# Kernel tuning notes

Measured on AMD Instinct MI355X. Metric: run time of the kernel, lower is better.

Reference implementation:

```python
import jax, jax.numpy as jnp
import numpy as np

N_NODES = 100000
N_EDGES = 800000
N_GRAPHS = 4000
EMB = 128      # node_emb_dims
HID = 256      # hidden_dims
FP = 2048      # fingerprint_dims
FIELD_DIMS = {"atom_type": 120, "degree": 12, "charge": 10}


def setup_inputs() -> dict:
    key = jax.random.key(0)
    ks = iter(jax.random.split(key, 40))
    p = lambda shape: jax.random.normal(next(ks), shape, dtype=jnp.float32) * 0.02
    inp = {
        "atom_idx": jax.random.randint(next(ks), (N_NODES,), 0, FIELD_DIMS["atom_type"]),
        "degree_idx": jax.random.randint(next(ks), (N_NODES,), 0, FIELD_DIMS["degree"]),
        "charge_idx": jax.random.randint(next(ks), (N_NODES,), 0, FIELD_DIMS["charge"]),
        "edge_index": jax.random.randint(next(ks), (2, N_EDGES), 0, N_NODES),
        "batch": jnp.sort(jax.random.randint(next(ks), (N_NODES,), 0, N_GRAPHS)),
        "fingerprint": jax.random.normal(next(ks), (N_GRAPHS, FP), dtype=jnp.float32),
        # FFM projector params
        "emb_atom": p((FIELD_DIMS["atom_type"], EMB)),
        "emb_degree": p((FIELD_DIMS["degree"], EMB)),
        "emb_charge": p((FIELD_DIMS["charge"], EMB)),
        "proj_w1": p((3 * EMB, EMB)), "proj_b1": jnp.zeros((EMB,), jnp.float32),
        "proj_w2": p((EMB, EMB)), "proj_b2": jnp.zeros((EMB,), jnp.float32),
        # fingerprint linear
        "fp_w": p((FP, HID)), "fp_b": jnp.zeros((HID,), jnp.float32),
        # GCN layers
        "conv_w0": p((EMB, HID)), "conv_b0": jnp.zeros((HID,), jnp.float32),
        "conv_w1": p((HID, HID)), "conv_b1": jnp.zeros((HID,), jnp.float32),
        "conv_w2": p((HID, HID)), "conv_b2": jnp.zeros((HID,), jnp.float32),
        "conv_w3": p((HID, HID)), "conv_b3": jnp.zeros((HID,), jnp.float32),
        # head
        "lin1_w": p((2 * HID, HID // 2)), "lin1_b": jnp.zeros((HID // 2,), jnp.float32),
        "lin2_w": p((HID // 2, 1)), "lin2_b": jnp.zeros((1,), jnp.float32),
    }
    return inp


def gcn_conv(x, w, b, src, dst, n):
    # PyG GCNConv: linear, add self-loops, symmetric norm, scatter-add at dst, + bias
    xw = x @ w
    loop = jnp.arange(n)
    src_f = jnp.concatenate([src, loop])
    dst_f = jnp.concatenate([dst, loop])
    deg = jax.ops.segment_sum(jnp.ones_like(dst_f, dtype=x.dtype), dst_f, num_segments=n)
    dinv = jax.lax.rsqrt(deg)  # deg >= 1 thanks to self-loops
    norm = dinv[src_f] * dinv[dst_f]                       # [E+N]
    msg = xw[src_f] * norm[:, None]                        # [E+N, HID]
    return jax.ops.segment_sum(msg, dst_f, num_segments=n) + b


def reference(atom_idx, degree_idx, charge_idx, edge_index, batch, fingerprint,
              emb_atom, emb_degree, emb_charge,
              proj_w1, proj_b1, proj_w2, proj_b2, fp_w, fp_b,
              conv_w0, conv_b0, conv_w1, conv_b1, conv_w2, conv_b2, conv_w3, conv_b3,
              lin1_w, lin1_b, lin2_w, lin2_b):
    # FieldAwareFactorizationMachine projector (vectorized over all nodes)
    e = jnp.concatenate([emb_atom[atom_idx], emb_degree[degree_idx], emb_charge[charge_idx]], axis=-1)
    h = jax.nn.relu(e @ proj_w1 + proj_b1) @ proj_w2 + proj_b2   # [N, EMB]
    src, dst = edge_index[0], edge_index[1]
    for w, b in ((conv_w0, conv_b0), (conv_w1, conv_b1), (conv_w2, conv_b2), (conv_w3, conv_b3)):
        h = jax.nn.relu(gcn_conv(h, w, b, src, dst, N_NODES))
    pooled = jax.ops.segment_sum(h, batch, num_segments=N_GRAPHS)  # scatter sum pooling
    fp_emb = fingerprint @ fp_w + fp_b
    z = jnp.concatenate([fp_emb, pooled], axis=-1)                 # [B, 2*HID]
    z = jax.nn.relu(z @ lin1_w + lin1_b)
    return z @ lin2_w + lin2_b                                     # [B, 1]
```

## Files before the change

### kernel.cpp

```cpp
#include <hip/hip_runtime.h>
#include <stdint.h>

#define NN 100000
#define NE 800000
#define NG 4000
#define NBLK ((NN + 255) / 256)

typedef __attribute__((ext_vector_type(8))) short s16x8;
typedef __attribute__((ext_vector_type(4))) float f32x4;

__device__ __forceinline__ float b2f(unsigned short u) {
    return __uint_as_float(((unsigned int)u) << 16);
}
__device__ __forceinline__ unsigned short f2b(float f) {
    unsigned int x = __float_as_uint(f);
    x = x + 0x7FFFu + ((x >> 16) & 1u);
    return (unsigned short)(x >> 16);
}
__device__ __forceinline__ s16x8 cvt8(const float* __restrict__ p) {
    float4 a = *(const float4*)p;
    float4 b = *(const float4*)(p + 4);
    s16x8 r = {(short)f2b(a.x), (short)f2b(a.y), (short)f2b(a.z), (short)f2b(a.w),
               (short)f2b(b.x), (short)f2b(b.y), (short)f2b(b.z), (short)f2b(b.w)};
    return r;
}

__global__ void k_count(const int* __restrict__ dst, int* __restrict__ cnt) {
    int e = blockIdx.x * 256 + threadIdx.x;
    if (e < NE) atomicAdd(&cnt[dst[e]], 1);
}

__global__ void k_dinv(const int* __restrict__ cnt, float* __restrict__ dinv) {
    int n = blockIdx.x * 256 + threadIdx.x;
    if (n < NN) dinv[n] = rsqrtf((float)(cnt[n] + 1));
}

__global__ __launch_bounds__(256) void k_bsum(const int* __restrict__ cnt, int* __restrict__ bsum) {
    __shared__ int s[256];
    int i = blockIdx.x * 256 + threadIdx.x;
    s[threadIdx.x] = (i < NN) ? cnt[i] : 0;
    __syncthreads();
    for (int off = 128; off; off >>= 1) {
        if (threadIdx.x < off) s[threadIdx.x] += s[threadIdx.x + off];
        __syncthreads();
    }
    if (threadIdx.x == 0) bsum[blockIdx.x] = s[0];
}

__global__ __launch_bounds__(512) void k_bscan(const int* __restrict__ bsum, int* __restrict__ bpre) {
    __shared__ int s[512];
    int t = threadIdx.x;
    int v = (t < NBLK) ? bsum[t] : 0;
    s[t] = v;
    __syncthreads();
    for (int off = 1; off < 512; off <<= 1) {
        int u = (t >= off) ? s[t - off] : 0;
        __syncthreads();
        s[t] += u;
        __syncthreads();
    }
    if (t < NBLK) bpre[t] = s[t] - v;
}

__global__ __launch_bounds__(256) void k_rowptr(const int* __restrict__ cnt, const int* __restrict__ bpre,
                                                int* __restrict__ row_ptr, int* __restrict__ cursor) {
    __shared__ int s[256];
    int t = threadIdx.x;
    int i = blockIdx.x * 256 + t;
    int v = (i < NN) ? cnt[i] : 0;
    s[t] = v;
    __syncthreads();
    for (int off = 1; off < 256; off <<= 1) {
        int u = (t >= off) ? s[t - off] : 0;
        __syncthreads();
        s[t] += u;
        __syncthreads();
    }
    if (i < NN) {
        int excl = bpre[blockIdx.x] + s[t] - v;
        row_ptr[i] = excl;
        cursor[i] = excl;
        if (i == NN - 1) row_ptr[NN] = NE;
    }
}

__global__ void k_fill(const int* __restrict__ src, const int* __restrict__ dst,
                       int* __restrict__ cursor, int* __restrict__ colA) {
    int e = blockIdx.x * 256 + threadIdx.x;
    if (e < NE) {
        int d = dst[e];
        int p = atomicAdd(&cursor[d], 1);
        colA[p] = src[e];
    }
}

__global__ void k_t(const float* __restrict__ src, unsigned short* __restrict__ dst, int KN, int ln) {
    int i = blockIdx.x * 256 + threadIdx.x;
    if (i < KN) {
        int k = i >> ln, n = i & ((1 << ln) - 1);
        dst[(size_t)n * (KN >> ln) + k] = f2b(src[i]);
    }
}

__global__ void k_cvt(const float* __restrict__ src, unsigned short* __restrict__ dst, int n8) {
    int i = blockIdx.x * 256 + threadIdx.x;
    if (i < n8) *(s16x8*)&dst[(size_t)i * 8] = cvt8(&src[(size_t)i * 8]);
}

template <bool GATHER, bool BIAS, bool RELU, bool CBF16>
__global__ __launch_bounds__(256) void k_mm(
    const unsigned short* __restrict__ A, const unsigned short* __restrict__ Bt,
    void* __restrict__ Cv, const float* __restrict__ bias, int M, int N, int K,
    const int* __restrict__ ai, const int* __restrict__ di, const int* __restrict__ ci,
    const float* __restrict__ ea, const float* __restrict__ ed, const float* __restrict__ ec) {
    __shared__ unsigned short As[128 * 40];
    __shared__ unsigned short Bs[128 * 40];
    const int tid = threadIdx.x;
    const int row0 = blockIdx.x * 128, col0 = blockIdx.y * 128;
    const int lane = tid & 63, wid = tid >> 6;
    const int wrow = (wid >> 1) * 64, wcol = (wid & 1) * 64;
    const int lr = lane & 15, lk8 = (lane >> 4) * 8;

    const int sr = tid >> 1;
    const int skc = (tid & 1) * 16;
    const int agrow = row0 + sr;
    const int bgrow = col0 + sr;
    int ia = 0, idg = 0, ic = 0;
    if (GATHER && agrow < M) { ia = ai[agrow] * 128; idg = di[agrow] * 128; ic = ci[agrow] * 128; }

    f32x4 acc[4][4] = {};

    for (int kb = 0; kb < K; kb += 32) {
        if (kb) __syncthreads();
#pragma unroll
        for (int c = 0; c < 2; ++c) {
            int kloc = skc + c * 8;
            s16x8 v = {};
            if (agrow < M) {
                if (GATHER) {
                    int kg = kb + kloc;
                    const float* p = (kg < 128) ? (ea + ia + kg)
                                   : (kg < 256) ? (ed + idg + kg - 128)
                                                : (ec + ic + kg - 256);
                    v = cvt8(p);
                } else {
                    v = *(const s16x8*)&A[(size_t)agrow * K + kb + kloc];
                }
            }
            *(s16x8*)&As[sr * 40 + kloc] = v;
            s16x8 w = *(const s16x8*)&Bt[(size_t)bgrow * K + kb + kloc];
            *(s16x8*)&Bs[sr * 40 + kloc] = w;
        }
        __syncthreads();
        s16x8 af[4], bfr[4];
#pragma unroll
        for (int f = 0; f < 4; ++f)
            af[f] = *(const s16x8*)&As[(wrow + f * 16 + lr) * 40 + lk8];
#pragma unroll
        for (int f = 0; f < 4; ++f)
            bfr[f] = *(const s16x8*)&Bs[(wcol + f * 16 + lr) * 40 + lk8];
#pragma unroll
        for (int fm = 0; fm < 4; ++fm)
#pragma unroll
            for (int fn = 0; fn < 4; ++fn)
                acc[fm][fn] = __builtin_amdgcn_mfma_f32_16x16x32_bf16(af[fm], bfr[fn], acc[fm][fn], 0, 0, 0);
    }
#pragma unroll
    for (int fm = 0; fm < 4; ++fm) {
#pragma unroll
        for (int r = 0; r < 4; ++r) {
            int row = row0 + wrow + fm * 16 + (lane >> 4) * 4 + r;
            if (row < M) {
#pragma unroll
                for (int fn = 0; fn < 4; ++fn) {
                    int col = col0 + wcol + fn * 16 + lr;
                    float v = acc[fm][fn][r];
                    if (BIAS) v += bias[col];
                    if (RELU) v = fmaxf(v, 0.f);
                    if (CBF16) ((unsigned short*)Cv)[(size_t)row * N + col] = f2b(v);
                    else       ((float*)Cv)[(size_t)row * N + col] = v;
                }
            }
        }
    }
}

template <int W, bool FUSE>
__global__ __launch_bounds__(256) void k_scat(const unsigned short* __restrict__ xw,
                                              unsigned short* __restrict__ hout,
                                              const float* __restrict__ dinv,
                                              const int* __restrict__ row_ptr,
                                              const int* __restrict__ colA,
                                              const float* __restrict__ bias) {
    constexpr int RPW = 1024 / W;
    constexpr int G = 64 / RPW;
    const int wid = threadIdx.x >> 6, lane = threadIdx.x & 63;
    const int v = blockIdx.x * 4 + wid;
    const int grp = lane / G, li = lane % G;
    const int c0 = li * 8;
    const float dv = dinv[v];
    float acc[8] = {};
    const int beg = row_ptr[v], end = row_ptr[v + 1];
    int p = beg + grp;
    for (; p + RPW < end; p += 2 * RPW) {
        int s0 = colA[p], s1 = colA[p + RPW];
        float w0 = dinv[s0] * dv, w1 = dinv[s1] * dv;
        s16x8 r0 = *(const s16x8*)&xw[(size_t)s0 * W + c0];
        s16x8 r1 = *(const s16x8*)&xw[(size_t)s1 * W + c0];
#pragma unroll
        for (int j = 0; j < 8; ++j) acc[j] = fmaf(b2f((unsigned short)r0[j]), w0, acc[j]);
#pragma unroll
        for (int j = 0; j < 8; ++j) acc[j] = fmaf(b2f((unsigned short)r1[j]), w1, acc[j]);
    }
    if (p < end) {
        int s0 = colA[p];
        float w0 = dinv[s0] * dv;
        s16x8 r0 = *(const s16x8*)&xw[(size_t)s0 * W + c0];
#pragma unroll
        for (int j = 0; j < 8; ++j) acc[j] = fmaf(b2f((unsigned short)r0[j]), w0, acc[j]);
    }
#pragma unroll
    for (int j = 0; j < 8; ++j) {
        if (RPW == 4) acc[j] += __shfl_xor(acc[j], 16);
        acc[j] += __shfl_xor(acc[j], 32);
    }
    s16x8 rs = *(const s16x8*)&xw[(size_t)v * W + c0];
    const float ws = dv * dv;
    unsigned short o[8];
#pragma unroll
    for (int j = 0; j < 8; ++j) {
        float x = fmaf(b2f((unsigned short)rs[j]), ws, acc[j]);
        if (FUSE) x = fmaxf(x + bias[c0 + j], 0.f);
        o[j] = f2b(x);
    }
    if (grp == 0) *(s16x8*)&hout[(size_t)v * W + c0] = *(const s16x8*)o;
}

__global__ void k_bounds(const int* __restrict__ batch, int* __restrict__ gstart) {
    int n = blockIdx.x * 256 + threadIdx.x;
    if (n >= NN) return;
    int b = batch[n];
    if (n == 0) {
        for (int g = 0; g <= b; ++g) gstart[g] = 0;
    } else {
        int pb = batch[n - 1];
        if (pb != b)
            for (int g = pb + 1; g <= b; ++g) gstart[g] = n;
    }
    if (n == NN - 1) {
        for (int g = b + 1; g <= NG; ++g) gstart[g] = NN;
    }
}

__global__ __launch_bounds__(64) void k_pool(const unsigned short* __restrict__ h,
                                             const int* __restrict__ gstart,
                                             float* __restrict__ pooled) {
    int g = blockIdx.x;
    int lane = threadIdx.x;
    int c0 = lane * 4;
    int beg = gstart[g], end = gstart[g + 1];
    float a0 = 0.f, a1 = 0.f, a2 = 0.f, a3 = 0.f;
    for (int n = beg; n < end; ++n) {
        ushort4 r = *(const ushort4*)&h[(size_t)n * 256 + c0];
        a0 += b2f(r.x); a1 += b2f(r.y); a2 += b2f(r.z); a3 += b2f(r.w);
    }
    float4 o; o.x = a0; o.y = a1; o.z = a2; o.w = a3;
    *(float4*)&pooled[(size_t)g * 256 + c0] = o;
}

__global__ __launch_bounds__(128) void k_head(const float* __restrict__ fp_emb,
                                              const float* __restrict__ pooled,
                                              const float* __restrict__ w1,
                                              const float* __restrict__ b1,
                                              const float* __restrict__ w2,
                                              const float* __restrict__ b2,
                                              float* __restrict__ out) {
    __shared__ float cat[512];
    __shared__ float red[128];
    int g = blockIdx.x, t = threadIdx.x;
    for (int i = t; i < 256; i += 128) cat[i] = fp_emb[(size_t)g * 256 + i];
    for (int i = t; i < 256; i += 128) cat[256 + i] = pooled[(size_t)g * 256 + i];
    __syncthreads();
    float s = b1[t];
    for (int i = 0; i < 512; ++i) s = fmaf(cat[i], w1[i * 128 + t], s);
    s = fmaxf(s, 0.f);
    red[t] = s * w2[t];
    __syncthreads();
    for (int off = 64; off > 0; off >>= 1) {
        if (t < off) red[t] += red[t + off];
        __syncthreads();
    }
    if (t == 0) out[g] = red[0] + b2[0];
}

extern "C" void kernel_launch(void* const* d_in, const int* in_sizes, int n_in,
                              void* d_out, int out_size, void* d_ws, size_t ws_size,
                              hipStream_t stream) {
    const int* atom_idx   = (const int*)d_in[0];
    const int* degree_idx = (const int*)d_in[1];
    const int* charge_idx = (const int*)d_in[2];
    const int* edge_index = (const int*)d_in[3];
    const int* batch      = (const int*)d_in[4];
    const float* fingerprint = (const float*)d_in[5];
    const float* emb_atom   = (const float*)d_in[6];
    const float* emb_degree = (const float*)d_in[7];
    const float* emb_charge = (const float*)d_in[8];
    const float* proj_w1 = (const float*)d_in[9];
    const float* proj_b1 = (const float*)d_in[10];
    const float* proj_w2 = (const float*)d_in[11];
    const float* proj_b2 = (const float*)d_in[12];
    const float* fp_w = (const float*)d_in[13];
    const float* fp_b = (const float*)d_in[14];
    const float* conv_w[4] = {(const float*)d_in[15], (const float*)d_in[17],
                              (const float*)d_in[19], (const float*)d_in[21]};
    const float* conv_b[4] = {(const float*)d_in[16], (const float*)d_in[18],
                              (const float*)d_in[20], (const float*)d_in[22]};
    const float* lin1_w = (const float*)d_in[23];
    const float* lin1_b = (const float*)d_in[24];
    const float* lin2_w = (const float*)d_in[25];
    const float* lin2_b = (const float*)d_in[26];
    float* out = (float*)d_out;

    const int* src = edge_index;
    const int* dst = edge_index + NE;

    char* p = (char*)d_ws;
    auto carve = [&](size_t bytes) { void* r = (void*)p; p += (bytes + 255) & ~(size_t)255; return r; };
    unsigned short* bufA = (unsigned short*)carve((size_t)NN * 256 * 2);
    unsigned short* bufB = (unsigned short*)carve((size_t)NN * 256 * 2);
    int*   cnt     = (int*)carve((size_t)NN * 4);
    float* dinv    = (float*)carve((size_t)NN * 4);
    int*   row_ptr = (int*)carve((size_t)(NN + 1) * 4);
    int*   cursor  = (int*)carve((size_t)(NN + 1) * 4);
    int*   colA    = (int*)carve((size_t)NE * 4);
    int*   gstart  = (int*)carve((size_t)(NG + 1) * 4);
    float* pooled  = (float*)carve((size_t)NG * 256 * 4);
    float* fp_emb  = (float*)carve((size_t)NG * 256 * 4);
    int*   bsum    = (int*)carve((size_t)NBLK * 4);
    int*   bpre    = (int*)carve((size_t)NBLK * 4);
    unsigned short* w1t  = (unsigned short*)carve((size_t)128 * 384 * 2);
    unsigned short* w2t  = (unsigned short*)carve((size_t)128 * 128 * 2);
    unsigned short* cwt[4];
    cwt[0] = (unsigned short*)carve((size_t)256 * 128 * 2);
    for (int l = 1; l < 4; ++l) cwt[l] = (unsigned short*)carve((size_t)256 * 256 * 2);
    unsigned short* fpwt = (unsigned short*)carve((size_t)256 * 2048 * 2);
    unsigned short* fpbf = (unsigned short*)carve((size_t)NG * 2048 * 2);

    hipMemsetAsync(cnt, 0, (size_t)NN * 4, stream);
    k_count<<<(NE + 255) / 256, 256, 0, stream>>>(dst, cnt);
    k_dinv<<<(NN + 255) / 256, 256, 0, stream>>>(cnt, dinv);
    k_bsum<<<NBLK, 256, 0, stream>>>(cnt, bsum);
    k_bscan<<<1, 512, 0, stream>>>(bsum, bpre);
    k_rowptr<<<NBLK, 256, 0, stream>>>(cnt, bpre, row_ptr, cursor);
    k_fill<<<(NE + 255) / 256, 256, 0, stream>>>(src, dst, cursor, colA);

    k_t<<<(49152 + 255) / 256, 256, 0, stream>>>(proj_w1, w1t, 49152, 7);
    k_t<<<(16384 + 255) / 256, 256, 0, stream>>>(proj_w2, w2t, 16384, 7);
    k_t<<<(32768 + 255) / 256, 256, 0, stream>>>(conv_w[0], cwt[0], 32768, 8);
    for (int l = 1; l < 4; ++l)
        k_t<<<(65536 + 255) / 256, 256, 0, stream>>>(conv_w[l], cwt[l], 65536, 8);
    k_t<<<(524288 + 255) / 256, 256, 0, stream>>>(fp_w, fpwt, 524288, 8);
    k_cvt<<<(NG * 2048 / 8 + 255) / 256, 256, 0, stream>>>(fingerprint, fpbf, NG * 2048 / 8);

    const int mg = (NN + 127) / 128;

    k_mm<true, true, true, true><<<dim3(mg, 1), 256, 0, stream>>>(
        nullptr, w1t, bufA, proj_b1, NN, 128, 384,
        atom_idx, degree_idx, charge_idx, emb_atom, emb_degree, emb_charge);
    k_mm<false, true, false, true><<<dim3(mg, 1), 256, 0, stream>>>(
        bufA, w2t, bufB, proj_b2, NN, 128, 128,
        nullptr, nullptr, nullptr, nullptr, nullptr, nullptr);

    k_scat<128, false><<<NN / 4, 256, 0, stream>>>(bufB, bufA, dinv, row_ptr, colA, nullptr);
    k_mm<false, true, true, true><<<dim3(mg, 2), 256, 0, stream>>>(
        bufA, cwt[0], bufB, conv_b[0], NN, 256, 128,
        nullptr, nullptr, nullptr, nullptr, nullptr, nullptr);

    for (int l = 1; l < 4; ++l) {
        k_mm<false, false, false, true><<<dim3(mg, 2), 256, 0, stream>>>(
            bufB, cwt[l], bufA, nullptr, NN, 256, 256,
            nullptr, nullptr, nullptr, nullptr, nullptr, nullptr);
        k_scat<256, true><<<NN / 4, 256, 0, stream>>>(bufA, bufB, dinv, row_ptr, colA, conv_b[l]);
    }

    k_bounds<<<(NN + 255) / 256, 256, 0, stream>>>(batch, gstart);
    k_pool<<<NG, 64, 0, stream>>>(bufB, gstart, pooled);

    k_mm<false, true, false, false><<<dim3((NG + 127) / 128, 2), 256, 0, stream>>>(
        fpbf, fpwt, fp_emb, fp_b, NG, 256, 2048,
        nullptr, nullptr, nullptr, nullptr, nullptr, nullptr);

    k_head<<<NG, 128, 0, stream>>>(fp_emb, pooled, lin1_w, lin1_b, lin2_w, lin2_b, out);
}
```

Measured before the change: 741.0 us.

## Use direct global-to-LDS loads in GEMMs, split-K fp GEMM, MFMA head, wider scatter

Adds a GEMM variant, k_mmA, that fills LDS with global_load_lds instead of staging through registers, and uses it for every non-gather matmul. The fingerprint GEMM becomes split-K over four chunks with atomic fp32 accumulation into a bias-initialised buffer. The per-graph scalar head is replaced by a bf16 concat buffer, an MFMA GEMM for lin1 and a warp-shuffle dot product for lin2. A new 256-wide scatter kernel gives each node two waves. The costs are extra small kernels, atomic contention and nondeterminism in split-K, and bf16 rounding of the head inputs.

```diff
diff --git a/kernel.cpp b/kernel.cpp
--- a/kernel.cpp
+++ b/kernel.cpp
@@ -23,6 +23,11 @@
     s16x8 r = {(short)f2b(a.x), (short)f2b(a.y), (short)f2b(a.z), (short)f2b(a.w),
                (short)f2b(b.x), (short)f2b(b.y), (short)f2b(b.z), (short)f2b(b.w)};
     return r;
+}
+
+__device__ __forceinline__ void gload16(const void* g, void* l) {
+    __builtin_amdgcn_global_load_lds((const __attribute__((address_space(1))) unsigned int*)g,
+                                     (__attribute__((address_space(3))) unsigned int*)l, 16, 0, 0);
 }
 
 __global__ void k_count(const int* __restrict__ dst, int* __restrict__ cnt) {
@@ -105,6 +110,17 @@
 __global__ void k_cvt(const float* __restrict__ src, unsigned short* __restrict__ dst, int n8) {
     int i = blockIdx.x * 256 + threadIdx.x;
     if (i < n8) *(s16x8*)&dst[(size_t)i * 8] = cvt8(&src[(size_t)i * 8]);
+}
+
+__global__ void k_binit(float* __restrict__ fe, const float* __restrict__ b) {
+    int i = blockIdx.x * 256 + threadIdx.x;
+    fe[i] = b[i & 255];
+}
+
+__global__ void k_z(const float* __restrict__ fe, unsigned short* __restrict__ zcat) {
+    int i = blockIdx.x * 256 + threadIdx.x;
+    int g = i >> 8, c = i & 255;
+    zcat[(size_t)g * 512 + c] = f2b(fe[i]);
 }
 
 template <bool GATHER, bool BIAS, bool RELU, bool CBF16>
@@ -179,6 +195,78 @@
                     if (RELU) v = fmaxf(v, 0.f);
                     if (CBF16) ((unsigned short*)Cv)[(size_t)row * N + col] = f2b(v);
                     else       ((float*)Cv)[(size_t)row * N + col] = v;
+                }
+            }
+        }
+    }
+}
+
+template <bool BIAS, bool RELU, bool CBF16, bool SPLITK>
+__global__ __launch_bounds__(256) void k_mmA(
+    const unsigned short* __restrict__ A, const unsigned short* __restrict__ Bt,
+    void* __restrict__ Cv, const float* __restrict__ bias, int M, int N, int K, int kc) {
+    __shared__ unsigned short As[128 * 32];
+    __shared__ unsigned short Bs[128 * 32];
+    const int tid = threadIdx.x;
+    const int row0 = blockIdx.x * 128, col0 = blockIdx.y * 128;
+    const int lane = tid & 63, wid = tid >> 6;
+    const int wrow = (wid >> 1) * 64, wcol = (wid & 1) * 64;
+    const int lr = lane & 15, lk8 = (lane >> 4) * 8;
+
+    const int k0 = SPLITK ? blockIdx.z * kc : 0;
+    const int k1 = SPLITK ? k0 + kc : K;
+
+    const int sra = wid * 32 + (lane >> 2);
+    const int sca = (lane & 3) * 8;
+    const unsigned short* a0 = A + (size_t)min(row0 + sra, M - 1) * K + sca;
+    const unsigned short* a1 = A + (size_t)min(row0 + sra + 16, M - 1) * K + sca;
+    const unsigned short* b0 = Bt + (size_t)(col0 + sra) * K + sca;
+    const unsigned short* b1 = Bt + (size_t)(col0 + sra + 16) * K + sca;
+    unsigned short* lA0 = &As[(wid * 2 + 0) * 512];
+    unsigned short* lA1 = &As[(wid * 2 + 1) * 512];
+    unsigned short* lB0 = &Bs[(wid * 2 + 0) * 512];
+    unsigned short* lB1 = &Bs[(wid * 2 + 1) * 512];
+
+    f32x4 acc[4][4] = {};
+
+    for (int kb = k0; kb < k1; kb += 32) {
+        if (kb != k0) __syncthreads();
+        gload16(a0 + kb, lA0);
+        gload16(a1 + kb, lA1);
+        gload16(b0 + kb, lB0);
+        gload16(b1 + kb, lB1);
+        __syncthreads();
+        s16x8 af[4], bfr[4];
+#pragma unroll
+        for (int f = 0; f < 4; ++f)
+            af[f] = *(const s16x8*)&As[(wrow + f * 16 + lr) * 32 + lk8];
+#pragma unroll
+        for (int f = 0; f < 4; ++f)
+            bfr[f] = *(const s16x8*)&Bs[(wcol + f * 16 + lr) * 32 + lk8];
+#pragma unroll
+        for (int fm = 0; fm < 4; ++fm)
+#pragma unroll
+            for (int fn = 0; fn < 4; ++fn)
+                acc[fm][fn] = __builtin_amdgcn_mfma_f32_16x16x32_bf16(af[fm], bfr[fn], acc[fm][fn], 0, 0, 0);
+    }
+#pragma unroll
+    for (int fm = 0; fm < 4; ++fm) {
+#pragma unroll
+        for (int r = 0; r < 4; ++r) {
+            int row = row0 + wrow + fm * 16 + (lane >> 4) * 4 + r;
+            if (row < M) {
+#pragma unroll
+                for (int fn = 0; fn < 4; ++fn) {
+                    int col = col0 + wcol + fn * 16 + lr;
+                    float v = acc[fm][fn][r];
+                    if (SPLITK) {
+                        atomicAdd(&((float*)Cv)[(size_t)row * N + col], v);
+                    } else {
+                        if (BIAS) v += bias[col];
+                        if (RELU) v = fmaxf(v, 0.f);
+                        if (CBF16) ((unsigned short*)Cv)[(size_t)row * N + col] = f2b(v);
+                        else       ((float*)Cv)[(size_t)row * N + col] = v;
+                    }
                 }
             }
         }
@@ -236,6 +324,55 @@
     if (grp == 0) *(s16x8*)&hout[(size_t)v * W + c0] = *(const s16x8*)o;
 }
 
+__global__ __launch_bounds__(256) void k_scat256(const unsigned short* __restrict__ xw,
+                                                 unsigned short* __restrict__ hout,
+                                                 const float* __restrict__ dinv,
+                                                 const int* __restrict__ row_ptr,
+                                                 const int* __restrict__ colA,
+                                                 const float* __restrict__ bias) {
+    const int wid = threadIdx.x >> 6, lane = threadIdx.x & 63;
+    const int v = blockIdx.x * 2 + (wid >> 1);
+    const int cs = (wid & 1) * 128;
+    const int grp = lane >> 4, li = lane & 15;
+    const int c0 = cs + li * 8;
+    const float dv = dinv[v];
+    float acc[8] = {};
+    const int beg = row_ptr[v], end = row_ptr[v + 1];
+    int p = beg + grp;
+    for (; p + 4 < end; p += 8) {
+        int s0 = colA[p], s1 = colA[p + 4];
+        float w0 = dinv[s0] * dv, w1 = dinv[s1] * dv;
+        s16x8 r0 = *(const s16x8*)&xw[(size_t)s0 * 256 + c0];
+        s16x8 r1 = *(const s16x8*)&xw[(size_t)s1 * 256 + c0];
+#pragma unroll
+        for (int j = 0; j < 8; ++j) acc[j] = fmaf(b2f((unsigned short)r0[j]), w0, acc[j]);
+#pragma unroll
+        for (int j = 0; j < 8; ++j) acc[j] = fmaf(b2f((unsigned short)r1[j]), w1, acc[j]);
+    }
+    if (p < end) {
+        int s0 = colA[p];
+        float w0 = dinv[s0] * dv;
+        s16x8 r0 = *(const s16x8*)&xw[(size_t)s0 * 256 + c0];
+#pragma unroll
+        for (int j = 0; j < 8; ++j) acc[j] = fmaf(b2f((unsigned short)r0[j]), w0, acc[j]);
+    }
+#pragma unroll
+    for (int j = 0; j < 8; ++j) {
+        acc[j] += __shfl_xor(acc[j], 16);
+        acc[j] += __shfl_xor(acc[j], 32);
+    }
+    s16x8 rs = *(const s16x8*)&xw[(size_t)v * 256 + c0];
+    const float ws = dv * dv;
+    unsigned short o[8];
+#pragma unroll
+    for (int j = 0; j < 8; ++j) {
+        float x = fmaf(b2f((unsigned short)rs[j]), ws, acc[j]);
+        x = fmaxf(x + bias[c0 + j], 0.f);
+        o[j] = f2b(x);
+    }
+    if (grp == 0) *(s16x8*)&hout[(size_t)v * 256 + c0] = *(const s16x8*)o;
+}
+
 __global__ void k_bounds(const int* __restrict__ batch, int* __restrict__ gstart) {
     int n = blockIdx.x * 256 + threadIdx.x;
     if (n >= NN) return;
@@ -254,7 +391,7 @@
 
 __global__ __launch_bounds__(64) void k_pool(const unsigned short* __restrict__ h,
                                              const int* __restrict__ gstart,
-                                             float* __restrict__ pooled) {
+                                             unsigned short* __restrict__ zcat) {
     int g = blockIdx.x;
     int lane = threadIdx.x;
     int c0 = lane * 4;
@@ -264,33 +401,22 @@
         ushort4 r = *(const ushort4*)&h[(size_t)n * 256 + c0];
         a0 += b2f(r.x); a1 += b2f(r.y); a2 += b2f(r.z); a3 += b2f(r.w);
     }
-    float4 o; o.x = a0; o.y = a1; o.z = a2; o.w = a3;
-    *(float4*)&pooled[(size_t)g * 256 + c0] = o;
-}
-
-__global__ __launch_bounds__(128) void k_head(const float* __restrict__ fp_emb,
-                                              const float* __restrict__ pooled,
-                                              const float* __restrict__ w1,
-                                              const float* __restrict__ b1,
-                                              const float* __restrict__ w2,
-                                              const float* __restrict__ b2,
-                                              float* __restrict__ out) {
-    __shared__ float cat[512];
-    __shared__ float red[128];
-    int g = blockIdx.x, t = threadIdx.x;
-    for (int i = t; i < 256; i += 128) cat[i] = fp_emb[(size_t)g * 256 + i];
-    for (int i = t; i < 256; i += 128) cat[256 + i] = pooled[(size_t)g * 256 + i];
-    __syncthreads();
-    float s = b1[t];
-    for (int i = 0; i < 512; ++i) s = fmaf(cat[i], w1[i * 128 + t], s);
-    s = fmaxf(s, 0.f);
-    red[t] = s * w2[t];
-    __syncthreads();
-    for (int off = 64; off > 0; off >>= 1) {
-        if (t < off) red[t] += red[t + off];
-        __syncthreads();
-    }
-    if (t == 0) out[g] = red[0] + b2[0];
+    ushort4 o;
+    o.x = f2b(a0); o.y = f2b(a1); o.z = f2b(a2); o.w = f2b(a3);
+    *(ushort4*)&zcat[(size_t)g * 512 + 256 + c0] = o;
+}
+
+__global__ __launch_bounds__(256) void k_dot(const float* __restrict__ z1,
+                                             const float* __restrict__ w2,
+                                             const float* __restrict__ b2,
+                                             float* __restrict__ out) {
+    int wid = threadIdx.x >> 6, lane = threadIdx.x & 63;
+    int g = blockIdx.x * 4 + wid;
+    float s = z1[(size_t)g * 128 + lane] * w2[lane]
+            + z1[(size_t)g * 128 + 64 + lane] * w2[64 + lane];
+#pragma unroll
+    for (int off = 32; off; off >>= 1) s += __shfl_xor(s, off);
+    if (lane == 0) out[g] = s + b2[0];
 }
 
 extern "C" void kernel_launch(void* const* d_in, const int* in_sizes, int n_in,
@@ -334,7 +460,6 @@
     int*   cursor  = (int*)carve((size_t)(NN + 1) * 4);
     int*   colA    = (int*)carve((size_t)NE * 4);
     int*   gstart  = (int*)carve((size_t)(NG + 1) * 4);
-    float* pooled  = (float*)carve((size_t)NG * 256 * 4);
     float* fp_emb  = (float*)carve((size_t)NG * 256 * 4);
     int*   bsum    = (int*)carve((size_t)NBLK * 4);
     int*   bpre    = (int*)carve((size_t)NBLK * 4);
@@ -345,6 +470,9 @@
     for (int l = 1; l < 4; ++l) cwt[l] = (unsigned short*)carve((size_t)256 * 256 * 2);
     unsigned short* fpwt = (unsigned short*)carve((size_t)256 * 2048 * 2);
     unsigned short* fpbf = (unsigned short*)carve((size_t)NG * 2048 * 2);
+    unsigned short* l1wt = (unsigned short*)carve((size_t)128 * 512 * 2);
+    unsigned short* zcat = (unsigned short*)carve((size_t)NG * 512 * 2);
+    float* z1      = (float*)carve((size_t)NG * 128 * 4);
 
     hipMemsetAsync(cnt, 0, (size_t)NN * 4, stream);
     k_count<<<(NE + 255) / 256, 256, 0, stream>>>(dst, cnt);
@@ -360,35 +488,36 @@
     for (int l = 1; l < 4; ++l)
         k_t<<<(65536 + 255) / 256, 256, 0, stream>>>(conv_w[l], cwt[l], 65536, 8);
     k_t<<<(524288 + 255) / 256, 256, 0, stream>>>(fp_w, fpwt, 524288, 8);
+    k_t<<<(65536 + 255) / 256, 256, 0, stream>>>(lin1_w, l1wt, 65536, 7);
     k_cvt<<<(NG * 2048 / 8 + 255) / 256, 256, 0, stream>>>(fingerprint, fpbf, NG * 2048 / 8);
+
+    k_binit<<<NG, 256, 0, stream>>>(fp_emb, fp_b);
+    k_mmA<false, false, false, true><<<dim3((NG + 127) / 128, 2, 4), 256, 0, stream>>>(
+        fpbf, fpwt, fp_emb, nullptr, NG, 256, 2048, 512);
+    k_z<<<NG, 256, 0, stream>>>(fp_emb, zcat);
 
     const int mg = (NN + 127) / 128;
 
     k_mm<true, true, true, true><<<dim3(mg, 1), 256, 0, stream>>>(
         nullptr, w1t, bufA, proj_b1, NN, 128, 384,
         atom_idx, degree_idx, charge_idx, emb_atom, emb_degree, emb_charge);
-    k_mm<false, true, false, true><<<dim3(mg, 1), 256, 0, stream>>>(
-        bufA, w2t, bufB, proj_b2, NN, 128, 128,
-        nullptr, nullptr, nullptr, nullptr, nullptr, nullptr);
+    k_mmA<true, false, true, false><<<dim3(mg, 1), 256, 0, stream>>>(
+        bufA, w2t, bufB, proj_b2, NN, 128, 128, 0);
 
     k_scat<128, false><<<NN / 4, 256, 0, stream>>>(bufB, bufA, dinv, row_ptr, colA, nullptr);
-    k_mm<false, true, true, true><<<dim3(mg, 2), 256, 0, stream>>>(
-        bufA, cwt[0], bufB, conv_b[0], NN, 256, 128,
-        nullptr, nullptr, nullptr, nullptr, nullptr, nullptr);
+    k_mmA<true, true, true, false><<<dim3(mg, 2), 256, 0, stream>>>(
+        bufA, cwt[0], bufB, conv_b[0], NN, 256, 128, 0);
 
     for (int l = 1; l < 4; ++l) {
-        k_mm<false, false, false, true><<<dim3(mg, 2), 256, 0, stream>>>(
-            bufB, cwt[l], bufA, nullptr, NN, 256, 256,
-            nullptr, nullptr, nullptr, nullptr, nullptr, nullptr);
-        k_scat<256, true><<<NN / 4, 256, 0, stream>>>(bufA, bufB, dinv, row_ptr, colA, conv_b[l]);
+        k_mmA<false, false, true, false><<<dim3(mg, 2), 256, 0, stream>>>(
+            bufB, cwt[l], bufA, nullptr, NN, 256, 256, 0);
+        k_scat256<<<NN / 2, 256, 0, stream>>>(bufA, bufB, dinv, row_ptr, colA, conv_b[l]);
     }
 
     k_bounds<<<(NN + 255) / 256, 256, 0, stream>>>(batch, gstart);
-    k_pool<<<NG, 64, 0, stream>>>(bufB, gstart, pooled);
-
-    k_mm<false, true, false, false><<<dim3((NG + 127) / 128, 2), 256, 0, stream>>>(
-        fpbf, fpwt, fp_emb, fp_b, NG, 256, 2048,
-        nullptr, nullptr, nullptr, nullptr, nullptr, nullptr);
-
-    k_head<<<NG, 128, 0, stream>>>(fp_emb, pooled, lin1_w, lin1_b, lin2_w, lin2_b, out);
-}
+    k_pool<<<NG, 64, 0, stream>>>(bufB, gstart, zcat);
+
+    k_mmA<true, true, false, false><<<dim3((NG + 127) / 128, 1), 256, 0, stream>>>(
+        zcat, l1wt, z1, lin1_b, NG, 128, 512, 0);
+    k_dot<<<NG / 4, 256, 0, stream>>>(z1, lin2_w, lin2_b, out);
+}
```

Result: slower. 805.7 us (+8.7%).
